# Kernel optimization log

Hardware: AMD Instinct MI355X
Metric: run time of the kernel (lower is better)

## Reference

```python
import jax, jax.numpy as jnp
import numpy as np

BN_EPS = 1e-5


def _bn(x, gamma, beta):
    # training-mode BatchNorm1d: biased batch stats over the edge/batch axis
    mean = jnp.mean(x, axis=0, keepdims=True)
    var = jnp.mean((x - mean) ** 2, axis=0, keepdims=True)
    return (x - mean) * jax.lax.rsqrt(var + BN_EPS) * gamma + beta


def setup_inputs() -> dict:
    key = jax.random.key(0)
    ks = jax.random.split(key, 20)
    N, E = 20000, 300000
    in_drug, in_prot, hidden = 256, 512, 256
    h2 = 2 * hidden

    def u(k, shape, fan_in):
        b = 1.0 / np.sqrt(fan_in)
        return jax.random.uniform(k, shape, jnp.float32, -b, b)

    return {
        "x_drug": jax.random.normal(ks[0], (N, in_drug), jnp.float32),
        "x_prot": jax.random.normal(ks[1], (N, in_prot), jnp.float32),
        "edge_index": jax.random.randint(ks[2], (2, E), 0, N, jnp.int64),
        "W_src": u(ks[3], (hidden, in_drug), in_drug),
        "W_dst": u(ks[4], (hidden, in_prot), in_prot),
        "W_gate": u(ks[5], (h2, h2), h2),
        "b_gate": u(ks[6], (h2,), h2),
        "W1": u(ks[7], (hidden, h2), h2),
        "b1": u(ks[8], (hidden,), h2),
        "g1": jnp.ones((hidden,), jnp.float32),
        "be1": jnp.zeros((hidden,), jnp.float32),
        "W2": u(ks[9], (hidden, hidden), hidden),
        "b2": u(ks[10], (hidden,), hidden),
        "g2": jnp.ones((hidden,), jnp.float32),
        "be2": jnp.zeros((hidden,), jnp.float32),
        "W3": u(ks[11], (1, hidden), hidden),
        "b3": u(ks[12], (1,), hidden),
        "W_bil": u(ks[13], (1, hidden, hidden), hidden),
        "b_bil": u(ks[14], (1,), hidden),
    }


def reference(x_drug, x_prot, edge_index, W_src, W_dst, W_gate, b_gate,
              W1, b1, g1, be1, W2, b2, g2, be2, W3, b3, W_bil, b_bil):
    src, dst = edge_index[0], edge_index[1]
    h_src = x_drug[src] @ W_src.T            # [E, H]
    h_dst = x_prot[dst] @ W_dst.T            # [E, H]
    h_cat = jnp.concatenate([h_src, h_dst], axis=1)  # [E, 2H]
    gate = jax.nn.sigmoid(h_cat @ W_gate.T + b_gate)
    h = gate * h_cat
    # MLP (dropout is identity here)
    h1 = jax.nn.relu(_bn(h @ W1.T + b1, g1, be1))
    h2_ = jax.nn.relu(_bn(h1 @ W2.T + b2, g2, be2))
    mlp_score = (h2_ @ W3.T + b3).reshape(-1)
    # Bilinear: out_ek = sum_ij h_src_ei W_kij h_dst_ej + b_k
    bil_score = (jnp.einsum("ei,kij,ej->ek", h_src, W_bil, h_dst) + b_bil).reshape(-1)
    return mlp_score + bil_score
```

## Files before the change

### kernel.cpp

```cpp
#include <hip/hip_runtime.h>
#include <hip/hip_bf16.h>

typedef unsigned short u16;
typedef __attribute__((ext_vector_type(8))) short bf16x8;
typedef __attribute__((ext_vector_type(8))) unsigned short us8;
typedef __attribute__((ext_vector_type(4))) float f32x4;


__device__ __forceinline__ float b2f(u16 u) {
    union { unsigned u32; float f; } x; x.u32 = ((unsigned)u) << 16; return x.f;
}
__device__ __forceinline__ u16 f2b(float f) {
    union { float f; unsigned u; } x; x.f = f;
    unsigned r = x.u + 0x7fffu + ((x.u >> 16) & 1u);
    return (u16)(r >> 16);
}

__global__ __launch_bounds__(256) void zero_kernel(float* p, int n) {
    int i = blockIdx.x * 256 + threadIdx.x;
    if (i < n) p[i] = 0.f;
}

struct CvtSeg { const float* in; u16* out; int n4; };
struct CvtArr { CvtSeg s[4]; int tot4; };
__global__ __launch_bounds__(256) void cvt_fused(CvtArr ca) {
    int i = blockIdx.x * 256 + threadIdx.x;
    if (i >= ca.tot4) return;
    int k = 0, off = i;
#pragma unroll
    for (int q = 0; q < 4; ++q) {
        if (off < ca.s[q].n4) { k = q; break; }
        off -= ca.s[q].n4;
    }
    float4 v = ((const float4*)ca.s[k].in)[off];
    ushort4 o; o.x = f2b(v.x); o.y = f2b(v.y); o.z = f2b(v.z); o.w = f2b(v.w);
    ((ushort4*)ca.s[k].out)[off] = o;
}

__global__ __launch_bounds__(256) void repack_swz(const float* __restrict__ W,
                                                  u16* __restrict__ out,
                                                  int total, int kbits) {
    int idx = blockIdx.x * 256 + threadIdx.x;
    if (idx >= total) return;
    const int n = idx >> kbits;
    const int k = idx & ((1 << kbits) - 1);
    const int ks = k >> 6, ke = k & 63;
    const int j = ke ^ ((n & 7) << 3);
    out[(((ks << 8) + n) << 6) + j] = f2b(W[idx]);
}

struct GDesc {
    const void* A; int lda; int a_f32;
    const u16* W; int ldb;
    u16* C; int ldc;
    int K;
    const float* bias;
};
template <int NY> struct GDescArr { GDesc d[NY]; };

template <int NY>
__global__ __launch_bounds__(256, 2) void mfma_node(GDescArr<NY> da, int M)
{
    const GDesc dd = da.d[blockIdx.y];
    __shared__ u16 As[2][128][40];
    __shared__ u16 Bs[2][256][40];
    const int t = threadIdx.x;
    const int row0 = blockIdx.x * 128;
    const int arow = t >> 1, aks = (t & 1) * 16;
    const int agr = min(row0 + arow, M - 1);
    const int w = t >> 6, lane = t & 63;
    const int wr = w >> 1, wc = w & 1;
    const int lrow = lane & 15, lkg = lane >> 4;
    const int NIT = dd.K >> 5;

    f32x4 acc[4][8] = {};
    us8 ar[2], br[4];
    float4 fr[4];

    auto load_regs = [&](int it) {
        const int k0 = it << 5;
        if (dd.a_f32) {
            const float* ap = (const float*)dd.A + (size_t)agr * dd.lda + k0 + aks;
#pragma unroll
            for (int q = 0; q < 4; ++q) fr[q] = *(const float4*)(ap + q * 4);
        } else {
            const u16* ap = (const u16*)dd.A + (size_t)agr * dd.lda + k0 + aks;
            ar[0] = *(const us8*)ap; ar[1] = *(const us8*)(ap + 8);
        }
        const u16* wp = dd.W + (size_t)t * dd.ldb + k0;
#pragma unroll
        for (int q = 0; q < 4; ++q) br[q] = *(const us8*)(wp + q * 8);
    };
    auto proc_write = [&](int b) {
        if (dd.a_f32) {
#pragma unroll
            for (int q = 0; q < 2; ++q) {
                us8 o;
                const float fq[8] = {fr[q*2].x, fr[q*2].y, fr[q*2].z, fr[q*2].w,
                                     fr[q*2+1].x, fr[q*2+1].y, fr[q*2+1].z, fr[q*2+1].w};
#pragma unroll
                for (int j = 0; j < 8; ++j) o[j] = f2b(fq[j]);
                *(us8*)&As[b][arow][aks + q * 8] = o;
            }
        } else {
            *(us8*)&As[b][arow][aks] = ar[0];
            *(us8*)&As[b][arow][aks + 8] = ar[1];
        }
#pragma unroll
        for (int q = 0; q < 4; ++q) *(us8*)&Bs[b][t][q * 8] = br[q];
    };
    auto do_mfma = [&](int b) {
        bf16x8 af[4];
#pragma unroll
        for (int mi = 0; mi < 4; ++mi)
            af[mi] = *(const bf16x8*)&As[b][wr * 64 + mi * 16 + lrow][lkg * 8];
#pragma unroll
        for (int ni = 0; ni < 8; ++ni) {
            bf16x8 bfr = *(const bf16x8*)&Bs[b][wc * 128 + ni * 16 + lrow][lkg * 8];
#pragma unroll
            for (int mi = 0; mi < 4; ++mi)
                acc[mi][ni] = __builtin_amdgcn_mfma_f32_16x16x32_bf16(
                    af[mi], bfr, acc[mi][ni], 0, 0, 0);
        }
    };

    load_regs(0); proc_write(0); __syncthreads();
    for (int it = 0; it < NIT; ++it) {
        const int cur = it & 1;
        if (it + 1 < NIT) load_regs(it + 1);
        do_mfma(cur);
        if (it + 1 < NIT) proc_write(cur ^ 1);
        __syncthreads();
    }

#pragma unroll
    for (int ni = 0; ni < 8; ++ni) {
        const int gcol = wc * 128 + ni * 16 + lrow;
        const float bv = dd.bias ? dd.bias[gcol] : 0.f;
#pragma unroll
        for (int mi = 0; mi < 4; ++mi) {
            f32x4 v = acc[mi][ni];
#pragma unroll
            for (int j = 0; j < 4; ++j) {
                const int grow = row0 + wr * 64 + mi * 16 + lkg * 4 + j;
                if (grow < M) dd.C[(size_t)grow * dd.ldc + gcol] = f2b(v[j] + bv);
            }
        }
    }
}

#define OP_GATE   1
#define OP_BNRELU 2

template <int AOP>
__global__ __launch_bounds__(256) void mfma_edge(
    const u16* __restrict__ Ain,
    const u16* __restrict__ Wb, int K,
    u16* __restrict__ C, int E,
    const int* __restrict__ ei,
    const u16* __restrict__ Gs, const u16* __restrict__ Gd,
    const u16* __restrict__ Hs, const u16* __restrict__ Hd,
    const u16* __restrict__ Bd, const float* __restrict__ b_bil,
    float* __restrict__ bil,
    const float* __restrict__ scaleK, const float* __restrict__ shiftK,
    float* __restrict__ sums)
{
    __shared__ u16 As[64][72];
    __shared__ u16 Bs[256 * 64];
    __shared__ float wsum[2][256];

    const int t = threadIdx.x;
    const int row0 = blockIdx.x * 64;
    const int arow = t >> 2;
    const int aks  = (t & 3) * 16;
    const int agr = min(row0 + arow, E - 1);

    int s_ = 0, d_ = 0;
    if constexpr (AOP == OP_GATE) { s_ = ei[agr]; d_ = ei[E + agr]; }

    const int lane = t & 63;
    const int w = t >> 6;
    const int lrow = lane & 15, lkg = lane >> 4;
    const int NKS = K >> 6;

    f32x4 acc[4][4] = {};
    float bdot = 0.f;
    us8 aw0, aw1;

    auto loadA = [&](int ks) {
        const int k = ks * 64 + aks;
        if constexpr (AOP == OP_GATE) {
            us8 gs0 = *(const us8*)(Gs + (size_t)s_ * 512 + k);
            us8 gs1 = *(const us8*)(Gs + (size_t)s_ * 512 + k + 8);
            us8 gd0 = *(const us8*)(Gd + (size_t)d_ * 512 + k);
            us8 gd1 = *(const us8*)(Gd + (size_t)d_ * 512 + k + 8);
            const u16* hp = (ks < 4) ? (Hs + (size_t)s_ * 256 + k)
                                     : (Hd + (size_t)d_ * 256 + k - 256);
            us8 h0 = *(const us8*)hp, h1 = *(const us8*)(hp + 8);
#pragma unroll
            for (int j = 0; j < 8; ++j) {
                const float x0 = b2f(gs0[j]) + b2f(gd0[j]);
                const float x1 = b2f(gs1[j]) + b2f(gd1[j]);
                const float r0 = __builtin_amdgcn_rcpf(1.f + __expf(-x0));
                const float r1 = __builtin_amdgcn_rcpf(1.f + __expf(-x1));
                aw0[j] = f2b(b2f(h0[j]) * r0);
                aw1[j] = f2b(b2f(h1[j]) * r1);
            }
            if (ks < 4) {
                us8 bd0 = *(const us8*)(Bd + (size_t)d_ * 256 + k);
                us8 bd1 = *(const us8*)(Bd + (size_t)d_ * 256 + k + 8);
#pragma unroll
                for (int j = 0; j < 8; ++j) {
                    bdot = fmaf(b2f(h0[j]), b2f(bd0[j]), bdot);
                    bdot = fmaf(b2f(h1[j]), b2f(bd1[j]), bdot);
                }
            }
        } else {
            us8 a0 = *(const us8*)(Ain + (size_t)agr * 256 + k);
            us8 a1 = *(const us8*)(Ain + (size_t)agr * 256 + k + 8);
            float4 c0 = *(const float4*)(scaleK + k);
            float4 c1 = *(const float4*)(scaleK + k + 4);
            float4 c2 = *(const float4*)(scaleK + k + 8);
            float4 c3 = *(const float4*)(scaleK + k + 12);
            float4 h0 = *(const float4*)(shiftK + k);
            float4 h1 = *(const float4*)(shiftK + k + 4);
            float4 h2 = *(const float4*)(shiftK + k + 8);
            float4 h3 = *(const float4*)(shiftK + k + 12);
            const float scq[16] = {c0.x,c0.y,c0.z,c0.w, c1.x,c1.y,c1.z,c1.w,
                                   c2.x,c2.y,c2.z,c2.w, c3.x,c3.y,c3.z,c3.w};
            const float shq[16] = {h0.x,h0.y,h0.z,h0.w, h1.x,h1.y,h1.z,h1.w,
                                   h2.x,h2.y,h2.z,h2.w, h3.x,h3.y,h3.z,h3.w};
#pragma unroll
            for (int j = 0; j < 8; ++j) {
                aw0[j] = f2b(fmaxf(fmaf(b2f(a0[j]), scq[j],     shq[j]),     0.f));
                aw1[j] = f2b(fmaxf(fmaf(b2f(a1[j]), scq[8 + j], shq[8 + j]), 0.f));
            }
        }
    };
    auto writeA = [&]() {
        *(us8*)&As[arow][aks]     = aw0;
        *(us8*)&As[arow][aks + 8] = aw1;
    };
    auto gloadB = [&](int ks) {
        const char* g = (const char*)(Wb + ((size_t)ks << 14)) + w * 8192 + lane * 16;
        char* l = (char*)Bs + w * 8192;
#pragma unroll
        for (int q = 0; q < 8; ++q)
            __builtin_amdgcn_global_load_lds(
                (const __attribute__((address_space(1))) unsigned int*)(g + q * 1024),
                (__attribute__((address_space(3))) unsigned int*)(l + q * 1024),
                16, 0, 0);
    };
    auto mfma_slab = [&]() {
#pragma unroll
        for (int kk = 0; kk < 64; kk += 32) {
            bf16x8 af[4], bf[4];
#pragma unroll
            for (int mi = 0; mi < 4; ++mi)
                af[mi] = *(const bf16x8*)&As[mi * 16 + lrow][kk + lkg * 8];
#pragma unroll
            for (int ni = 0; ni < 4; ++ni) {
                const int r = w * 64 + ni * 16 + lrow;
                bf[ni] = *(const bf16x8*)&Bs[r * 64 + ((kk + lkg * 8) ^ ((r & 7) << 3))];
            }
#pragma unroll
            for (int ni = 0; ni < 4; ++ni)
#pragma unroll
                for (int mi = 0; mi < 4; ++mi)
                    acc[mi][ni] = __builtin_amdgcn_mfma_f32_16x16x32_bf16(
                        af[mi], bf[ni], acc[mi][ni], 0, 0, 0);
        }
    };

    gloadB(0); loadA(0);
    for (int ks = 0; ks < NKS; ++ks) {
        writeA();
        __syncthreads();
        if (ks + 1 < NKS) loadA(ks + 1);
        mfma_slab();
        __syncthreads();
        if (ks + 1 < NKS) gloadB(ks + 1);
    }

    if constexpr (AOP == OP_GATE) {
        bdot += __shfl_xor(bdot, 1, 64);
        bdot += __shfl_xor(bdot, 2, 64);
        if ((t & 3) == 0 && row0 + arow < E)
            bil[row0 + arow] = bdot + b_bil[0];
    }

#pragma unroll
    for (int ni = 0; ni < 4; ++ni) {
        const int gcol = w * 64 + ni * 16 + lrow;
        float s = 0.f, ss = 0.f;
#pragma unroll
        for (int mi = 0; mi < 4; ++mi) {
            f32x4 v = acc[mi][ni];
#pragma unroll
            for (int j = 0; j < 4; ++j) {
                const int grow = row0 + mi * 16 + lkg * 4 + j;
                const float x = v[j];
                if (grow < E) {
                    C[(size_t)grow * 256 + gcol] = f2b(x);
                    s += x; ss = fmaf(x, x, ss);
                }
            }
        }
        s  += __shfl_xor(s, 16, 64);  s  += __shfl_xor(s, 32, 64);
        ss += __shfl_xor(ss, 16, 64); ss += __shfl_xor(ss, 32, 64);
        if (lkg == 0) { wsum[0][gcol] = s; wsum[1][gcol] = ss; }
    }
    __syncthreads();
    atomicAdd(&sums[t],       wsum[0][t]);
    atomicAdd(&sums[256 + t], wsum[1][t]);
}

__global__ void finalize_kernel(
    const float* __restrict__ sums, const float* __restrict__ g,
    const float* __restrict__ be, int M,
    float* __restrict__ scale, float* __restrict__ shift)
{
    const int c = threadIdx.x;
    const float inv = 1.f / (float)M;
    const float mean = sums[c] * inv;
    const float var  = sums[256 + c] * inv - mean * mean;
    const float sc = g[c] * rsqrtf(var + 1e-5f);
    scale[c] = sc;
    shift[c] = fmaf(-mean, sc, be[c]);
}

__global__ __launch_bounds__(256) void final_kernel(
    const u16* __restrict__ Z2,
    const float* __restrict__ scale2, const float* __restrict__ shift2,
    const float* __restrict__ W3, const float* __restrict__ b3,
    const float* __restrict__ bil,
    float* __restrict__ out, int E)
{
    const int w = threadIdx.x >> 6, lane = threadIdx.x & 63;
    const int e = blockIdx.x * 4 + w;
    if (e >= E) return;
    ushort4 zv = *(const ushort4*)(Z2 + (size_t)e * 256 + lane * 4);
    float4 sc = *(const float4*)(scale2 + lane * 4);
    float4 sh = *(const float4*)(shift2 + lane * 4);
    float4 w3 = *(const float4*)(W3 + lane * 4);
    const u16 zq[4] = {zv.x, zv.y, zv.z, zv.w};
    const float scq[4] = {sc.x, sc.y, sc.z, sc.w};
    const float shq[4] = {sh.x, sh.y, sh.z, sh.w};
    const float wq[4] = {w3.x, w3.y, w3.z, w3.w};
    float acc = 0.f;
#pragma unroll
    for (int i = 0; i < 4; ++i) {
        const float x = fmaxf(fmaf(b2f(zq[i]), scq[i], shq[i]), 0.f);
        acc = fmaf(x, wq[i], acc);
    }
#pragma unroll
    for (int off = 32; off; off >>= 1) acc += __shfl_down(acc, off, 64);
    if (lane == 0) out[e] = acc + b3[0] + bil[e];
}

extern "C" void kernel_launch(void* const* d_in, const int* in_sizes, int n_in,
                              void* d_out, int out_size, void* d_ws, size_t ws_size,
                              hipStream_t stream)
{
    const float* x_drug = (const float*)d_in[0];
    const float* x_prot = (const float*)d_in[1];
    const int*   ei     = (const int*)d_in[2];
    const float* W_src  = (const float*)d_in[3];
    const float* W_dst  = (const float*)d_in[4];
    const float* W_gate = (const float*)d_in[5];
    const float* b_gate = (const float*)d_in[6];
    const float* W1     = (const float*)d_in[7];
    const float* g1     = (const float*)d_in[9];
    const float* be1    = (const float*)d_in[10];
    const float* W2     = (const float*)d_in[11];
    const float* g2     = (const float*)d_in[13];
    const float* be2    = (const float*)d_in[14];
    const float* W3     = (const float*)d_in[15];
    const float* b3     = (const float*)d_in[16];
    const float* W_bil  = (const float*)d_in[17];
    const float* b_bil  = (const float*)d_in[18];
    float* out = (float*)d_out;

    const int N = in_sizes[0] / 256;
    const int E = in_sizes[2] / 2;

    char* wp_ = (char*)d_ws;
    auto alloc = [&](size_t bytes) {
        char* p = wp_; wp_ += (bytes + 255) & ~(size_t)255; return p;
    };
    u16* Wsrcb  = (u16*)alloc(256 * 256 * 2);
    u16* Wdstb  = (u16*)alloc(256 * 512 * 2);
    u16* Wgateb = (u16*)alloc(512 * 512 * 2);
    u16* Wbilb  = (u16*)alloc(256 * 256 * 2);
    u16* W1s    = (u16*)alloc(256 * 512 * 2);
    u16* W2s    = (u16*)alloc(256 * 256 * 2);
    u16* Hs     = (u16*)alloc((size_t)N * 256 * 2);
    u16* Hd     = (u16*)alloc((size_t)N * 256 * 2);
    u16* Gs     = (u16*)alloc((size_t)N * 512 * 2);
    u16* Gd     = (u16*)alloc((size_t)N * 512 * 2);
    u16* Bd     = (u16*)alloc((size_t)N * 256 * 2);
    u16* z      = (u16*)alloc((size_t)E * 256 * 2);
    float* bil  = (float*)alloc((size_t)E * 4);
    float* sums   = (float*)alloc(1024 * 4);
    float* scale1 = (float*)alloc(256 * 4);
    float* shift1 = (float*)alloc(256 * 4);
    float* scale2 = (float*)alloc(256 * 4);
    float* shift2 = (float*)alloc(256 * 4);

    zero_kernel<<<4, 256, 0, stream>>>(sums, 1024);

    CvtArr ca;
    ca.s[0] = {W_src,  Wsrcb,  256 * 256 / 4};
    ca.s[1] = {W_dst,  Wdstb,  256 * 512 / 4};
    ca.s[2] = {W_gate, Wgateb, 512 * 512 / 4};
    ca.s[3] = {W_bil,  Wbilb,  256 * 256 / 4};
    ca.tot4 = 0;
    for (int q = 0; q < 4; ++q) ca.tot4 += ca.s[q].n4;
    cvt_fused<<<(ca.tot4 + 255) / 256, 256, 0, stream>>>(ca);

    repack_swz<<<(256 * 512 + 255) / 256, 256, 0, stream>>>(W1, W1s, 256 * 512, 9);
    repack_swz<<<(256 * 256 + 255) / 256, 256, 0, stream>>>(W2, W2s, 256 * 256, 8);

    const int gxN = (N + 127) / 128;
    const int gxE = (E + 63) / 64;

    GDescArr<2> p1;
    p1.d[0] = {x_drug, 256, 1, Wsrcb, 256, Hs, 256, 256, nullptr};
    p1.d[1] = {x_prot, 512, 1, Wdstb, 512, Hd, 256, 512, nullptr};
    mfma_node<2><<<dim3(gxN, 2), 256, 0, stream>>>(p1, N);

    GDescArr<5> p2;
    p2.d[0] = {Hs, 256, 0, Wgateb,                 512, Gs,       512, 256, b_gate};
    p2.d[1] = {Hs, 256, 0, Wgateb + 256 * 512,     512, Gs + 256, 512, 256, b_gate + 256};
    p2.d[2] = {Hd, 256, 0, Wgateb + 256,           512, Gd,       512, 256, nullptr};
    p2.d[3] = {Hd, 256, 0, Wgateb + 256 * 512 + 256, 512, Gd + 256, 512, 256, nullptr};
    p2.d[4] = {Hd, 256, 0, Wbilb,                  256, Bd,       256, 256, nullptr};
    mfma_node<5><<<dim3(gxN, 5), 256, 0, stream>>>(p2, N);

    mfma_edge<OP_GATE><<<gxE, 256, 0, stream>>>(
        nullptr, W1s, 512, z, E,
        ei, Gs, Gd, Hs, Hd, Bd, b_bil, bil, nullptr, nullptr, sums);
    finalize_kernel<<<1, 256, 0, stream>>>(sums, g1, be1, E, scale1, shift1);

    mfma_edge<OP_BNRELU><<<gxE, 256, 0, stream>>>(
        z, W2s, 256, z, E,
        nullptr, nullptr, nullptr, nullptr, nullptr, nullptr, nullptr, nullptr,
        scale1, shift1, sums + 512);
    finalize_kernel<<<1, 256, 0, stream>>>(sums + 512, g2, be2, E, scale2, shift2);

    final_kernel<<<(E + 3) / 4, 256, 0, stream>>>(
        z, scale2, shift2, W3, b3, bil, out, E);
}
```

Measured before the change: 525.7 us.

## Sort edges by destination node to improve gather locality in edge GEMM

Adds a counting sort of the edges by destination node (histogram, single-block scan, atomic scatter) that produces permuted src/dst index arrays plus an inverse permutation. The gate edge kernel gathers Gd/Hd/Bd rows through the sorted order, so consecutive rows in a tile tend to share destination nodes and hit in cache. The final kernel writes each result back to its original edge slot. This adds four small launches and atomic traffic. The single-block scan over 20000 nodes runs serially per thread chunk and may add latency.

```diff
diff --git a/kernel.cpp b/kernel.cpp
--- a/kernel.cpp
+++ b/kernel.cpp
@@ -2,13 +2,14 @@
 #include <hip/hip_bf16.h>
 
 typedef unsigned short u16;
+typedef unsigned int u32;
 typedef __attribute__((ext_vector_type(8))) short bf16x8;
 typedef __attribute__((ext_vector_type(8))) unsigned short us8;
 typedef __attribute__((ext_vector_type(4))) float f32x4;
 
 
 __device__ __forceinline__ float b2f(u16 u) {
-    union { unsigned u32; float f; } x; x.u32 = ((unsigned)u) << 16; return x.f;
+    union { unsigned u32v; float f; } x; x.u32v = ((unsigned)u) << 16; return x.f;
 }
 __device__ __forceinline__ u16 f2b(float f) {
     union { float f; unsigned u; } x; x.f = f;
@@ -16,9 +17,9 @@
     return (u16)(r >> 16);
 }
 
-__global__ __launch_bounds__(256) void zero_kernel(float* p, int n) {
+__global__ __launch_bounds__(256) void zero_kernel(u32* p, int n) {
     int i = blockIdx.x * 256 + threadIdx.x;
-    if (i < n) p[i] = 0.f;
+    if (i < n) p[i] = 0u;
 }
 
 struct CvtSeg { const float* in; u16* out; int n4; };
@@ -47,6 +48,47 @@
     const int ks = k >> 6, ke = k & 63;
     const int j = ke ^ ((n & 7) << 3);
     out[(((ks << 8) + n) << 6) + j] = f2b(W[idx]);
+}
+
+__global__ __launch_bounds__(256) void hist_kernel(const int* __restrict__ ei,
+                                                   int E, u32* __restrict__ hist) {
+    int e = blockIdx.x * 256 + threadIdx.x;
+    if (e < E) atomicAdd(&hist[ei[E + e]], 1u);
+}
+
+__global__ __launch_bounds__(256) void scan_kernel(const u32* __restrict__ hist,
+                                                   u32* __restrict__ cursor, int n) {
+    __shared__ u32 part[256];
+    const int t = threadIdx.x;
+    const int chunk = (n + 255) / 256;
+    const int lo = t * chunk, hi = min(lo + chunk, n);
+    u32 s = 0;
+    for (int i = lo; i < hi; ++i) s += hist[i];
+    part[t] = s;
+    __syncthreads();
+    for (int off = 1; off < 256; off <<= 1) {
+        u32 v = (t >= off) ? part[t - off] : 0u;
+        __syncthreads();
+        part[t] += v;
+        __syncthreads();
+    }
+    u32 base = (t == 0) ? 0u : part[t - 1];
+    for (int i = lo; i < hi; ++i) {
+        cursor[i] = base;
+        base += hist[i];
+    }
+}
+
+__global__ __launch_bounds__(256) void scatter_kernel(const int* __restrict__ ei,
+                                                      int E, u32* __restrict__ cursor,
+                                                      int* __restrict__ se,
+                                                      int* __restrict__ de,
+                                                      int* __restrict__ pe) {
+    int e = blockIdx.x * 256 + threadIdx.x;
+    if (e >= E) return;
+    const int d = ei[E + e];
+    const u32 pos = atomicAdd(&cursor[d], 1u);
+    se[pos] = ei[e]; de[pos] = d; pe[pos] = e;
 }
 
 struct GDesc {
@@ -157,7 +199,7 @@
     const u16* __restrict__ Ain,
     const u16* __restrict__ Wb, int K,
     u16* __restrict__ C, int E,
-    const int* __restrict__ ei,
+    const int* __restrict__ se, const int* __restrict__ de,
     const u16* __restrict__ Gs, const u16* __restrict__ Gd,
     const u16* __restrict__ Hs, const u16* __restrict__ Hd,
     const u16* __restrict__ Bd, const float* __restrict__ b_bil,
@@ -176,7 +218,7 @@
     const int agr = min(row0 + arow, E - 1);
 
     int s_ = 0, d_ = 0;
-    if constexpr (AOP == OP_GATE) { s_ = ei[agr]; d_ = ei[E + agr]; }
+    if constexpr (AOP == OP_GATE) { s_ = se[agr]; d_ = de[agr]; }
 
     const int lane = t & 63;
     const int w = t >> 6;
@@ -333,7 +375,7 @@
     const u16* __restrict__ Z2,
     const float* __restrict__ scale2, const float* __restrict__ shift2,
     const float* __restrict__ W3, const float* __restrict__ b3,
-    const float* __restrict__ bil,
+    const float* __restrict__ bil, const int* __restrict__ pe,
     float* __restrict__ out, int E)
 {
     const int w = threadIdx.x >> 6, lane = threadIdx.x & 63;
@@ -355,7 +397,7 @@
     }
 #pragma unroll
     for (int off = 32; off; off >>= 1) acc += __shfl_down(acc, off, 64);
-    if (lane == 0) out[e] = acc + b3[0] + bil[e];
+    if (lane == 0) out[pe[e]] = acc + b3[0] + bil[e];
 }
 
 extern "C" void kernel_launch(void* const* d_in, const int* in_sizes, int n_in,
@@ -401,13 +443,23 @@
     u16* Bd     = (u16*)alloc((size_t)N * 256 * 2);
     u16* z      = (u16*)alloc((size_t)E * 256 * 2);
     float* bil  = (float*)alloc((size_t)E * 4);
+    u32*  hist  = (u32*)alloc((size_t)N * 4);
+    u32*  cursor= (u32*)alloc((size_t)N * 4);
+    int*  se    = (int*)alloc((size_t)E * 4);
+    int*  de    = (int*)alloc((size_t)E * 4);
+    int*  pe    = (int*)alloc((size_t)E * 4);
     float* sums   = (float*)alloc(1024 * 4);
     float* scale1 = (float*)alloc(256 * 4);
     float* shift1 = (float*)alloc(256 * 4);
     float* scale2 = (float*)alloc(256 * 4);
     float* shift2 = (float*)alloc(256 * 4);
 
-    zero_kernel<<<4, 256, 0, stream>>>(sums, 1024);
+    zero_kernel<<<4, 256, 0, stream>>>((u32*)sums, 1024);
+    zero_kernel<<<(N + 255) / 256, 256, 0, stream>>>(hist, N);
+
+    hist_kernel<<<(E + 255) / 256, 256, 0, stream>>>(ei, E, hist);
+    scan_kernel<<<1, 256, 0, stream>>>(hist, cursor, N);
+    scatter_kernel<<<(E + 255) / 256, 256, 0, stream>>>(ei, E, cursor, se, de, pe);
 
     CvtArr ca;
     ca.s[0] = {W_src,  Wsrcb,  256 * 256 / 4};
@@ -439,15 +491,15 @@
 
     mfma_edge<OP_GATE><<<gxE, 256, 0, stream>>>(
         nullptr, W1s, 512, z, E,
-        ei, Gs, Gd, Hs, Hd, Bd, b_bil, bil, nullptr, nullptr, sums);
+        se, de, Gs, Gd, Hs, Hd, Bd, b_bil, bil, nullptr, nullptr, sums);
     finalize_kernel<<<1, 256, 0, stream>>>(sums, g1, be1, E, scale1, shift1);
 
     mfma_edge<OP_BNRELU><<<gxE, 256, 0, stream>>>(
         z, W2s, 256, z, E,
         nullptr, nullptr, nullptr, nullptr, nullptr, nullptr, nullptr, nullptr,
-        scale1, shift1, sums + 512);
+        nullptr, scale1, shift1, sums + 512);
     finalize_kernel<<<1, 256, 0, stream>>>(sums + 512, g2, be2, E, scale2, shift2);
 
     final_kernel<<<(E + 3) / 4, 256, 0, stream>>>(
-        z, scale2, shift2, W3, b3, bil, out, E);
-}
+        z, scale2, shift2, W3, b3, bil, pe, out, E);
+}
```

Result: slower. 575.0 us (+9.4%).
